# Optimization experiments

Measured on AMD Instinct MI355X. Metric: run time of the kernel, lower is better.

## Reference

```python
import jax, jax.numpy as jnp
import numpy as np

N = 100000
E = 1600000
H = 128       # hidden_channels
HEADS = 8
HD = H // HEADS  # head_dim = 16


def setup_inputs() -> dict:
    key = jax.random.key(0)
    ks = jax.random.split(key, 10)
    x = jax.random.normal(ks[0], (N, H), dtype=jnp.float32)
    gap_edge_index = jax.random.randint(ks[1], (2, E), 0, N, dtype=jnp.int64)
    s = 1.0 / np.sqrt(H)
    Wq = jax.random.normal(ks[2], (H, H), dtype=jnp.float32) * s
    bq = jnp.zeros((H,), dtype=jnp.float32)
    Wk = jax.random.normal(ks[3], (H, H), dtype=jnp.float32) * s
    bk = jnp.zeros((H,), dtype=jnp.float32)
    Wv = jax.random.normal(ks[4], (H, H), dtype=jnp.float32) * s
    bv = jnp.zeros((H,), dtype=jnp.float32)
    Wo = jax.random.normal(ks[5], (H, H), dtype=jnp.float32) * s
    bo = jnp.zeros((H,), dtype=jnp.float32)
    return {"x": x, "gap_edge_index": gap_edge_index,
            "Wq": Wq, "bq": bq, "Wk": Wk, "bk": bk,
            "Wv": Wv, "bv": bv, "Wo": Wo, "bo": bo}


def reference(x, gap_edge_index, Wq, bq, Wk, bk, Wv, bv, Wo, bo):
    n = x.shape[0]
    q = (x @ Wq + bq).reshape(n, HEADS, HD)
    k = (x @ Wk + bk).reshape(n, HEADS, HD)
    v = (x @ Wv + bv).reshape(n, HEADS, HD)
    src, dst = gap_edge_index[0], gap_edge_index[1]
    # per-edge, per-head scores: [E, heads]
    scores = jnp.einsum('ehd,ehd->eh', q[dst], k[src]) / jnp.sqrt(jnp.float32(HD))
    # NOTE: original softmaxes over ALL edges (dim=0), not per-dst segment
    w = jax.nn.softmax(scores, axis=0)
    # scatter-add weighted v[src] into dst: [N, heads, head_dim]
    attended = jax.ops.segment_sum(w[:, :, None] * v[src], dst, num_segments=n)
    attended = attended.reshape(n, HEADS * HD)
    return x + attended @ Wo + bo
```

## Files before the change

### kernel.cpp

```cpp
#include <hip/hip_runtime.h>
#include <cstdint>
#include <cstddef>

#define N_NODES 100000
#define E_EDGES 1600000
#define HCH 128
#define NHEADS 8
#define HDIM 16

typedef unsigned int uint;
typedef unsigned short ushort;
typedef __attribute__((ext_vector_type(8))) short short8;
typedef __attribute__((ext_vector_type(4))) float floatx4;
typedef __attribute__((ext_vector_type(2))) float floatx2;

typedef unsigned char uchar;

constexpr int GTILES = (N_NODES + 63) / 64;

__device__ __forceinline__ ushort f2bf(float f) {
    uint u = __float_as_uint(f);
    u = (u + 0x7fff + ((u >> 16) & 1)) >> 16;
    return (ushort)u;
}
__device__ __forceinline__ float bflo(uint p) { return __uint_as_float(p << 16); }
__device__ __forceinline__ float bfhi(uint p) { return __uint_as_float(p & 0xffff0000u); }

__global__ __launch_bounds__(256) void prep_w(
    const float* __restrict__ Wq, const float* __restrict__ Wk,
    const float* __restrict__ Wv, const float* __restrict__ Wo,
    ushort* __restrict__ wall)
{
    const int t = threadIdx.x;
    int r = blockIdx.x * 16 + (t >> 4);
    int k0 = (t & 15) * 8;
    const float* W;
    if (r < 128)      W = Wq;
    else if (r < 256) W = Wk;
    else if (r < 384) W = Wv;
    else              W = Wo;
    int n = r & 127;
    uint4 u;
    u.x = (uint)f2bf(W[(size_t)(k0 + 0) * HCH + n]) | ((uint)f2bf(W[(size_t)(k0 + 1) * HCH + n]) << 16);
    u.y = (uint)f2bf(W[(size_t)(k0 + 2) * HCH + n]) | ((uint)f2bf(W[(size_t)(k0 + 3) * HCH + n]) << 16);
    u.z = (uint)f2bf(W[(size_t)(k0 + 4) * HCH + n]) | ((uint)f2bf(W[(size_t)(k0 + 5) * HCH + n]) << 16);
    u.w = (uint)f2bf(W[(size_t)(k0 + 6) * HCH + n]) | ((uint)f2bf(W[(size_t)(k0 + 7) * HCH + n]) << 16);
    *(uint4*)(wall + (size_t)r * HCH + k0) = u;
}

__global__ __launch_bounds__(256) void gemm_qkv(
    const float* __restrict__ A, const ushort* __restrict__ wall,
    const float* __restrict__ bq, const float* __restrict__ bk, const float* __restrict__ bv,
    uchar* __restrict__ qe, uchar* __restrict__ kb, uchar* __restrict__ vb,
    int M)
{
    __shared__ __align__(16) ushort Wt[128][136];
    __shared__ __align__(16) char smem[64 * 136 * 2];
    ushort (*As)[136] = (ushort(*)[136])smem;
    ushort (*Cs)[136] = (ushort(*)[136])smem;

    const int t = threadIdx.x;
    const int mode = blockIdx.x % 3;
    const int tile0 = blockIdx.x / 3;
    const float* bias;
    uchar* outp;
    if (mode == 0)      { bias = bq; outp = qe; }
    else if (mode == 1) { bias = bk; outp = kb; }
    else                { bias = bv; outp = vb; }

#pragma unroll
    for (int i = 0; i < 8; i++) {
        int p = t + i * 256;
        int row = p >> 4, k0 = (p & 15) * 8;
        *(uint4*)(&Wt[row][k0]) =
            *(const uint4*)(wall + ((size_t)(mode * 128 + row)) * HCH + k0);
    }

    const int lane = t & 63;
    const int w = t >> 6;
    const int m_l = lane & 15;
    const int q_l = lane >> 4;

    for (int tile = tile0; tile < GTILES; tile += 256) {
        const int mb = tile * 64;
#pragma unroll
        for (int i = 0; i < 8; i++) {
            int p = t + i * 256;
            int row = p >> 5, c4 = p & 31;
            int g = mb + row;
            float4 a4 = make_float4(0.f, 0.f, 0.f, 0.f);
            if (g < M) a4 = *(const float4*)(A + (size_t)g * HCH + c4 * 4);
            uint lo = (uint)f2bf(a4.x) | ((uint)f2bf(a4.y) << 16);
            uint hi = (uint)f2bf(a4.z) | ((uint)f2bf(a4.w) << 16);
            *(uint2*)(&As[row][c4 * 4]) = make_uint2(lo, hi);
        }
        __syncthreads();

        floatx4 acc[8];
#pragma unroll
        for (int tl = 0; tl < 8; tl++) acc[tl] = (floatx4){0.f, 0.f, 0.f, 0.f};
#pragma unroll
        for (int ks = 0; ks < 4; ks++) {
            short8 af = *(const short8*)(&As[w * 16 + m_l][ks * 32 + q_l * 8]);
#pragma unroll
            for (int tl = 0; tl < 8; tl++) {
                short8 bf = *(const short8*)(&Wt[tl * 16 + m_l][ks * 32 + q_l * 8]);
                acc[tl] = __builtin_amdgcn_mfma_f32_16x16x32_bf16(af, bf, acc[tl], 0, 0, 0);
            }
        }
        __syncthreads();

#pragma unroll
        for (int tl = 0; tl < 8; tl++)
#pragma unroll
            for (int r = 0; r < 4; r++)
                Cs[w * 16 + q_l * 4 + r][tl * 16 + m_l] = f2bf(acc[tl][r]);
        __syncthreads();

#pragma unroll
        for (int i = 0; i < 4; i++) {
            int p = t + i * 256;
            int row = p >> 4, u = p & 15;
            int g = mb + row;
            if (g < M) {
                uint4 c = *(const uint4*)(&Cs[row][u * 8]);
                float4 b0 = *(const float4*)(bias + u * 8);
                float4 b1 = *(const float4*)(bias + u * 8 + 4);
                int r0 = __builtin_amdgcn_cvt_pk_fp8_f32(bflo(c.x) + b0.x, bfhi(c.x) + b0.y, 0, false);
                r0 = __builtin_amdgcn_cvt_pk_fp8_f32(bflo(c.y) + b0.z, bfhi(c.y) + b0.w, r0, true);
                int r1 = __builtin_amdgcn_cvt_pk_fp8_f32(bflo(c.z) + b1.x, bfhi(c.z) + b1.y, 0, false);
                r1 = __builtin_amdgcn_cvt_pk_fp8_f32(bflo(c.w) + b1.z, bfhi(c.w) + b1.w, r1, true);
                *(uint2*)(outp + (size_t)g * 128 + u * 8) = make_uint2((uint)r0, (uint)r1);
            }
        }
        __syncthreads();
    }
}

__global__ __launch_bounds__(256) void gemm_out(
    const ushort* __restrict__ A, const ushort* __restrict__ wall,
    const float* __restrict__ bias, const float* __restrict__ res,
    const float* __restrict__ head_invl,
    float* __restrict__ C, int M)
{
    __shared__ __align__(16) ushort Wt[128][136];
    __shared__ __align__(16) char smem[64 * 136 * 2];
    ushort (*As)[136] = (ushort(*)[136])smem;
    ushort (*Cs)[136] = (ushort(*)[136])smem;

    const int t = threadIdx.x;

    __shared__ float invl_s[8];
    if (t < 8) invl_s[t] = head_invl[t];

#pragma unroll
    for (int i = 0; i < 8; i++) {
        int p = t + i * 256;
        int row = p >> 4, k0 = (p & 15) * 8;
        *(uint4*)(&Wt[row][k0]) =
            *(const uint4*)(wall + ((size_t)(384 + row)) * HCH + k0);
    }

    const int lane = t & 63;
    const int w = t >> 6;
    const int m_l = lane & 15;
    const int q_l = lane >> 4;

    for (int tile = blockIdx.x; tile < GTILES; tile += 768) {
        const int mb = tile * 64;
#pragma unroll
        for (int i = 0; i < 8; i++) {
            int p = t + i * 256;
            int row = p >> 5, cu2 = p & 31;
            int g = mb + row;
            uint2 a = make_uint2(0, 0);
            if (g < M) a = *(const uint2*)(A + (size_t)g * HCH + cu2 * 4);
            float invl = invl_s[cu2 >> 2];
            float f0 = bflo(a.x) * invl, f1 = bfhi(a.x) * invl;
            float f2 = bflo(a.y) * invl, f3 = bfhi(a.y) * invl;
            uint lo = (uint)f2bf(f0) | ((uint)f2bf(f1) << 16);
            uint hi = (uint)f2bf(f2) | ((uint)f2bf(f3) << 16);
            *(uint2*)(&As[row][cu2 * 4]) = make_uint2(lo, hi);
        }
        __syncthreads();

        floatx4 acc[8];
#pragma unroll
        for (int tl = 0; tl < 8; tl++) acc[tl] = (floatx4){0.f, 0.f, 0.f, 0.f};
#pragma unroll
        for (int ks = 0; ks < 4; ks++) {
            short8 af = *(const short8*)(&As[w * 16 + m_l][ks * 32 + q_l * 8]);
#pragma unroll
            for (int tl = 0; tl < 8; tl++) {
                short8 bf = *(const short8*)(&Wt[tl * 16 + m_l][ks * 32 + q_l * 8]);
                acc[tl] = __builtin_amdgcn_mfma_f32_16x16x32_bf16(af, bf, acc[tl], 0, 0, 0);
            }
        }
        __syncthreads();

#pragma unroll
        for (int tl = 0; tl < 8; tl++)
#pragma unroll
            for (int r = 0; r < 4; r++)
                Cs[w * 16 + q_l * 4 + r][tl * 16 + m_l] = f2bf(acc[tl][r]);
        __syncthreads();

#pragma unroll
        for (int i = 0; i < 8; i++) {
            int p = t + i * 256;
            int row = p >> 5, u = p & 31;
            int g = mb + row;
            if (g < M) {
                uint2 c = *(const uint2*)(&Cs[row][u * 4]);
                float4 b4 = *(const float4*)(bias + u * 4);
                float4 r4 = *(const float4*)(res + (size_t)g * HCH + u * 4);
                float4 o;
                o.x = bflo(c.x) + b4.x + r4.x;
                o.y = bfhi(c.x) + b4.y + r4.y;
                o.z = bflo(c.y) + b4.z + r4.z;
                o.w = bfhi(c.y) + b4.w + r4.w;
                *(float4*)(C + (size_t)g * HCH + u * 4) = o;
            }
        }
        __syncthreads();
    }
}

constexpr int BSHIFT = 8;
constexpr int NBUCK  = ((N_NODES - 1) >> BSHIFT) + 1;
constexpr int S1_GRID = 256;
constexpr int S1_CH   = (E_EDGES + S1_GRID - 1) / S1_GRID;
constexpr int S2_CAP  = 6144;

__global__ __launch_bounds__(256) void bucket_hist(
    const int* __restrict__ dst, int* __restrict__ bucket_total)
{
    __shared__ int cnt[NBUCK];
    const int t = threadIdx.x;
    for (int b = t; b < NBUCK; b += 256) cnt[b] = 0;
    __syncthreads();
    const int e0 = blockIdx.x * S1_CH;
    const int n = min(S1_CH, E_EDGES - e0);
    for (int i = t; i < n; i += 256)
        atomicAdd(&cnt[dst[e0 + i] >> BSHIFT], 1);
    __syncthreads();
    for (int b = t; b < NBUCK; b += 256)
        if (cnt[b]) atomicAdd(&bucket_total[b], cnt[b]);
}

__global__ __launch_bounds__(512) void bucket_scan(
    const int* __restrict__ bucket_total, int* __restrict__ bucket_start,
    int* __restrict__ bucket_cursor, int* __restrict__ offsets)
{
    __shared__ int s[512];
    const int t = threadIdx.x;
    int v = (t < NBUCK) ? bucket_total[t] : 0;
    s[t] = v;
    __syncthreads();
    for (int off = 1; off < 512; off <<= 1) {
        int a = (t >= off) ? s[t - off] : 0;
        __syncthreads();
        s[t] += a;
        __syncthreads();
    }
    int excl = s[t] - v;
    if (t < NBUCK) { bucket_start[t] = excl; bucket_cursor[t] = excl; }
    if (t == 0) { bucket_start[NBUCK] = E_EDGES; offsets[N_NODES] = E_EDGES; }
}

__global__ __launch_bounds__(256) void sort_scatter1(
    const int* __restrict__ src, const int* __restrict__ dst,
    int* __restrict__ bucket_cursor, int2* __restrict__ tmp)
{
    __shared__ int ls[S1_CH];
    __shared__ int ld[S1_CH];
    __shared__ int cnt[NBUCK];
    const int t = threadIdx.x;
    for (int b = t; b < NBUCK; b += 256) cnt[b] = 0;
    __syncthreads();
    const int e0 = blockIdx.x * S1_CH;
    const int n = min(S1_CH, E_EDGES - e0);
    for (int i = t; i < n; i += 256) {
        int d = dst[e0 + i];
        ls[i] = src[e0 + i];
        ld[i] = d;
        atomicAdd(&cnt[d >> BSHIFT], 1);
    }
    __syncthreads();
    for (int b = t; b < NBUCK; b += 256) {
        int c = cnt[b];
        cnt[b] = c ? atomicAdd(&bucket_cursor[b], c) : 0;
    }
    __syncthreads();
    for (int i = t; i < n; i += 256) {
        int d = ld[i];
        int pos = atomicAdd(&cnt[d >> BSHIFT], 1);
        tmp[pos] = make_int2(ls[i], d);
    }
}

__global__ __launch_bounds__(256) void sort_scatter2(
    const int2* __restrict__ tmp, const int* __restrict__ bucket_start,
    int* __restrict__ psrc, int* __restrict__ offsets)
{
    __shared__ int2 le[S2_CAP];
    __shared__ int cnt[256];
    __shared__ int s[256];
    __shared__ int cur[256];
    const int t = threadIdx.x;
    const int b = blockIdx.x;
    const int bstart = bucket_start[b];
    const int n = bucket_start[b + 1] - bstart;
    cnt[t] = 0;
    __syncthreads();
    for (int i = t; i < n; i += 256) {
        int2 e = tmp[bstart + i];
        if (i < S2_CAP) le[i] = e;
        atomicAdd(&cnt[e.y & 255], 1);
    }
    __syncthreads();
    int v = cnt[t];
    s[t] = v;
    __syncthreads();
    for (int off = 1; off < 256; off <<= 1) {
        int a = (t >= off) ? s[t - off] : 0;
        __syncthreads();
        s[t] += a;
        __syncthreads();
    }
    int excl = s[t] - v;
    int node = (b << BSHIFT) + t;
    if (node < N_NODES) offsets[node] = bstart + excl;
    cur[t] = excl;
    __syncthreads();
    for (int i = t; i < n; i += 256) {
        int2 e = (i < S2_CAP) ? le[i] : tmp[bstart + i];
        int pos = bstart + atomicAdd(&cur[e.y & 255], 1);
        psrc[pos] = e.x;
    }
}

constexpr int FU_BLOCKS = 2048;
constexpr int FU_GROUPS = FU_BLOCKS * 16;

__device__ __forceinline__ float edge_w(
    uint2 e, floatx2 q0, floatx2 q1, floatx2 q2, floatx2 q3)
{
    floatx2 dp = q0 * __builtin_amdgcn_cvt_pk_f32_fp8((int)e.x, false);
    dp += q1 * __builtin_amdgcn_cvt_pk_f32_fp8((int)e.x, true);
    dp += q2 * __builtin_amdgcn_cvt_pk_f32_fp8((int)e.y, false);
    dp += q3 * __builtin_amdgcn_cvt_pk_f32_fp8((int)e.y, true);
    float p = dp.x + dp.y;
    p += __shfl_xor(p, 1);
    return __expf(p * 0.25f);
}
__device__ __forceinline__ void edge_acc(
    uint2 e, float wgt, floatx2& a01, floatx2& a23, floatx2& a45, floatx2& a67)
{
    floatx2 wv = {wgt, wgt};
    a01 += wv * __builtin_amdgcn_cvt_pk_f32_fp8((int)e.x, false);
    a23 += wv * __builtin_amdgcn_cvt_pk_f32_fp8((int)e.x, true);
    a45 += wv * __builtin_amdgcn_cvt_pk_f32_fp8((int)e.y, false);
    a67 += wv * __builtin_amdgcn_cvt_pk_f32_fp8((int)e.y, true);
}

__global__ __launch_bounds__(256) void edge_fused(
    const uchar* __restrict__ qe, const uchar* __restrict__ kb, const uchar* __restrict__ vb,
    const int* __restrict__ psrc, const int* __restrict__ offsets,
    ushort* __restrict__ attended, float* __restrict__ block_l)
{
    const int t = threadIdx.x;
    const int sub = t & 15;
    const int gg0 = blockIdx.x * 16 + (t >> 4);

    float lsum = 0.f;

    for (int d = gg0; d < N_NODES; d += FU_GROUPS) {
        const int start = offsets[d];
        const int end   = offsets[d + 1];

        uint2 qw = *(const uint2*)(qe + (size_t)d * 128 + sub * 8);
        floatx2 q0 = __builtin_amdgcn_cvt_pk_f32_fp8((int)qw.x, false);
        floatx2 q1 = __builtin_amdgcn_cvt_pk_f32_fp8((int)qw.x, true);
        floatx2 q2 = __builtin_amdgcn_cvt_pk_f32_fp8((int)qw.y, false);
        floatx2 q3 = __builtin_amdgcn_cvt_pk_f32_fp8((int)qw.y, true);

        floatx2 a01 = {0.f, 0.f}, a23 = {0.f, 0.f}, a45 = {0.f, 0.f}, a67 = {0.f, 0.f};

        for (int i = start; i < end; i += 4) {
            int i1 = min(i + 1, end - 1);
            int i2 = min(i + 2, end - 1);
            int i3 = min(i + 3, end - 1);
            int s0 = psrc[i];
            int s1 = psrc[i1];
            int s2 = psrc[i2];
            int s3 = psrc[i3];
            uint2 k0 = *(const uint2*)(kb + (size_t)s0 * 128 + sub * 8);
            uint2 k1 = *(const uint2*)(kb + (size_t)s1 * 128 + sub * 8);
            uint2 k2 = *(const uint2*)(kb + (size_t)s2 * 128 + sub * 8);
            uint2 k3 = *(const uint2*)(kb + (size_t)s3 * 128 + sub * 8);
            uint2 v0 = *(const uint2*)(vb + (size_t)s0 * 128 + sub * 8);
            uint2 v1 = *(const uint2*)(vb + (size_t)s1 * 128 + sub * 8);
            uint2 v2 = *(const uint2*)(vb + (size_t)s2 * 128 + sub * 8);
            uint2 v3 = *(const uint2*)(vb + (size_t)s3 * 128 + sub * 8);

            float w0 = edge_w(k0, q0, q1, q2, q3);
            float w1 = edge_w(k1, q0, q1, q2, q3);
            float w2 = edge_w(k2, q0, q1, q2, q3);
            float w3 = edge_w(k3, q0, q1, q2, q3);
            if (i + 1 >= end) w1 = 0.f;
            if (i + 2 >= end) w2 = 0.f;
            if (i + 3 >= end) w3 = 0.f;
            lsum += w0 + w1 + w2 + w3;

            edge_acc(v0, w0, a01, a23, a45, a67);
            edge_acc(v1, w1, a01, a23, a45, a67);
            edge_acc(v2, w2, a01, a23, a45, a67);
            edge_acc(v3, w3, a01, a23, a45, a67);
        }

        uint4 o;
        o.x = (uint)f2bf(a01.x) | ((uint)f2bf(a01.y) << 16);
        o.y = (uint)f2bf(a23.x) | ((uint)f2bf(a23.y) << 16);
        o.z = (uint)f2bf(a45.x) | ((uint)f2bf(a45.y) << 16);
        o.w = (uint)f2bf(a67.x) | ((uint)f2bf(a67.y) << 16);
        *(uint4*)(attended + (size_t)d * HCH + sub * 8) = o;
    }

    __shared__ float sl[256];
    sl[t] = lsum;
    __syncthreads();
    if (t < 8) {
        float L = 0.f;
        for (int base = 0; base < 256; base += 16)
            L += sl[base + 2 * t] + sl[base + 2 * t + 1];
        block_l[blockIdx.x * 8 + t] = 0.5f * L;
    }
}

__global__ __launch_bounds__(256) void reduce_l(
    const float* __restrict__ block_l, float* __restrict__ head_invl, int nblk)
{
    const int t = threadIdx.x;
    float l = 0.f;
    for (int i = t; i < nblk * 8; i += 256) l += block_l[i];
    __shared__ float sl[256];
    sl[t] = l;
    __syncthreads();
    if (t < 8) {
        float L = 0.f;
        for (int i = t; i < 256; i += 8) L += sl[i];
        head_invl[t] = 1.0f / L;
    }
}

extern "C" void kernel_launch(void* const* d_in, const int* in_sizes, int n_in,
                              void* d_out, int out_size, void* d_ws, size_t ws_size,
                              hipStream_t stream)
{
    const float* x  = (const float*)d_in[0];
    const int* eidx = (const int*)d_in[1];
    const float* Wq = (const float*)d_in[2];
    const float* bq = (const float*)d_in[3];
    const float* Wk = (const float*)d_in[4];
    const float* bk = (const float*)d_in[5];
    const float* Wv = (const float*)d_in[6];
    const float* bv = (const float*)d_in[7];
    const float* Wo = (const float*)d_in[8];
    const float* bo = (const float*)d_in[9];
    float* out = (float*)d_out;

    char* ws = (char*)d_ws;
    constexpr size_t SZ_F8  = (size_t)N_NODES * HCH;
    constexpr size_t SZ_ATT = (size_t)N_NODES * HCH * 2;
    constexpr size_t SZ_PS  = (size_t)E_EDGES * sizeof(int);
    constexpr size_t SZ_TMP = (size_t)E_EDGES * sizeof(int2);
    size_t off = 0;
    uchar* qe = (uchar*)(ws + off); off += SZ_F8;
    uchar* kb = (uchar*)(ws + off); off += SZ_F8;
    uchar* vb = (uchar*)(ws + off); off += SZ_F8;
    ushort* attended = (ushort*)(ws + off); off += SZ_ATT;
    int*    psrc     = (int*)(ws + off);    off += SZ_PS;
    int2*   tmp      = (int2*)(ws + off);   off += SZ_TMP;
    int*    offsets  = (int*)(ws + off);    off += ((size_t)N_NODES + 1) * 4 + 8;
    int*    bucket_total  = (int*)(ws + off); off += (NBUCK + 1) * 4;
    int*    bucket_start  = (int*)(ws + off); off += (NBUCK + 1) * 4;
    int*    bucket_cursor = (int*)(ws + off); off += (NBUCK + 1) * 4;
    float*  block_l   = (float*)(ws + off); off += (size_t)FU_BLOCKS * 8 * sizeof(float);
    float*  head_invl = (float*)(ws + off); off += 32;
    ushort* wall = (ushort*)(ws + off); off += (size_t)512 * HCH * 2;
    const int* src = eidx;
    const int* dst = eidx + E_EDGES;

    dim3 blk(256);

    prep_w<<<32, blk, 0, stream>>>(Wq, Wk, Wv, Wo, wall);

    gemm_qkv<<<768, blk, 0, stream>>>(x, wall, bq, bk, bv, qe, kb, vb, N_NODES);

    hipMemsetAsync(bucket_total, 0, (NBUCK + 1) * 4, stream);
    bucket_hist<<<S1_GRID, blk, 0, stream>>>(dst, bucket_total);
    bucket_scan<<<1, 512, 0, stream>>>(bucket_total, bucket_start, bucket_cursor, offsets);
    sort_scatter1<<<S1_GRID, blk, 0, stream>>>(src, dst, bucket_cursor, tmp);
    sort_scatter2<<<NBUCK, blk, 0, stream>>>(tmp, bucket_start, psrc, offsets);

    edge_fused<<<FU_BLOCKS, blk, 0, stream>>>(qe, kb, vb, psrc, offsets, attended, block_l);
    reduce_l<<<1, blk, 0, stream>>>(block_l, head_invl, FU_BLOCKS);

    gemm_out<<<768, blk, 0, stream>>>(attended, wall, bo, x, head_invl, out, N_NODES);
}
```

Measured before the change: 335.4 us.

## Fuse QKV GEMM with edge scatter, pack sort temp, prefetch tiles, drop launches

Merges the QKV projection GEMM and the first sort-scatter pass into one launch, with different block ranges doing different work so the two overlap. The sort temp is packed from int2 into a single uint holding the source id plus the low 8 bits of dst. Both GEMMs now register-prefetch the next A tile, and the edge loop double-buffers its K/V gathers. The memset and the reduce_l kernel are removed: bucket zeroing moves into prep_w and the softmax normaliser reduction moves into every gemm_out block. The trade-offs are redundant per-block reduction work and more register pressure. The packing also assumes source ids fit in 17 bits.

```diff
diff --git a/kernel.cpp b/kernel.cpp
--- a/kernel.cpp
+++ b/kernel.cpp
@@ -10,11 +10,10 @@
 
 typedef unsigned int uint;
 typedef unsigned short ushort;
+typedef unsigned char uchar;
 typedef __attribute__((ext_vector_type(8))) short short8;
 typedef __attribute__((ext_vector_type(4))) float floatx4;
 typedef __attribute__((ext_vector_type(2))) float floatx2;
-
-typedef unsigned char uchar;
 
 constexpr int GTILES = (N_NODES + 63) / 64;
 
@@ -26,12 +25,23 @@
 __device__ __forceinline__ float bflo(uint p) { return __uint_as_float(p << 16); }
 __device__ __forceinline__ float bfhi(uint p) { return __uint_as_float(p & 0xffff0000u); }
 
+constexpr int BSHIFT = 8;
+constexpr int NBUCK  = ((N_NODES - 1) >> BSHIFT) + 1;
+constexpr int S1_GRID = 256;
+constexpr int S1_CH   = (E_EDGES + S1_GRID - 1) / S1_GRID;
+constexpr int S2_CAP  = 6144;
+constexpr int FU_BLOCKS = 2048;
+constexpr int FU_GROUPS = FU_BLOCKS * 16;
+
 __global__ __launch_bounds__(256) void prep_w(
     const float* __restrict__ Wq, const float* __restrict__ Wk,
     const float* __restrict__ Wv, const float* __restrict__ Wo,
-    ushort* __restrict__ wall)
-{
-    const int t = threadIdx.x;
+    ushort* __restrict__ wall, int* __restrict__ bucket_total)
+{
+    const int t = threadIdx.x;
+    if (blockIdx.x == 0) {
+        for (int b = t; b < NBUCK + 1; b += 256) bucket_total[b] = 0;
+    }
     int r = blockIdx.x * 16 + (t >> 4);
     int k0 = (t & 15) * 8;
     const float* W;
@@ -48,20 +58,84 @@
     *(uint4*)(wall + (size_t)r * HCH + k0) = u;
 }
 
-__global__ __launch_bounds__(256) void gemm_qkv(
+__global__ __launch_bounds__(256) void bucket_hist(
+    const int* __restrict__ dst, int* __restrict__ bucket_total)
+{
+    __shared__ int cnt[NBUCK];
+    const int t = threadIdx.x;
+    for (int b = t; b < NBUCK; b += 256) cnt[b] = 0;
+    __syncthreads();
+    const int e0 = blockIdx.x * S1_CH;
+    const int n = min(S1_CH, E_EDGES - e0);
+    for (int i = t; i < n; i += 256)
+        atomicAdd(&cnt[dst[e0 + i] >> BSHIFT], 1);
+    __syncthreads();
+    for (int b = t; b < NBUCK; b += 256)
+        if (cnt[b]) atomicAdd(&bucket_total[b], cnt[b]);
+}
+
+__global__ __launch_bounds__(512) void bucket_scan(
+    const int* __restrict__ bucket_total, int* __restrict__ bucket_start,
+    int* __restrict__ bucket_cursor, int* __restrict__ offsets)
+{
+    __shared__ int s[512];
+    const int t = threadIdx.x;
+    int v = (t < NBUCK) ? bucket_total[t] : 0;
+    s[t] = v;
+    __syncthreads();
+    for (int off = 1; off < 512; off <<= 1) {
+        int a = (t >= off) ? s[t - off] : 0;
+        __syncthreads();
+        s[t] += a;
+        __syncthreads();
+    }
+    int excl = s[t] - v;
+    if (t < NBUCK) { bucket_start[t] = excl; bucket_cursor[t] = excl; }
+    if (t == 0) { bucket_start[NBUCK] = E_EDGES; offsets[N_NODES] = E_EDGES; }
+}
+
+__global__ __launch_bounds__(256) void mega_qkv_scatter(
     const float* __restrict__ A, const ushort* __restrict__ wall,
     const float* __restrict__ bq, const float* __restrict__ bk, const float* __restrict__ bv,
     uchar* __restrict__ qe, uchar* __restrict__ kb, uchar* __restrict__ vb,
+    const int* __restrict__ src, const int* __restrict__ dst,
+    int* __restrict__ bucket_cursor, uint* __restrict__ tmp,
     int M)
 {
-    __shared__ __align__(16) ushort Wt[128][136];
-    __shared__ __align__(16) char smem[64 * 136 * 2];
-    ushort (*As)[136] = (ushort(*)[136])smem;
-    ushort (*Cs)[136] = (ushort(*)[136])smem;
-
-    const int t = threadIdx.x;
-    const int mode = blockIdx.x % 3;
-    const int tile0 = blockIdx.x / 3;
+    __shared__ __align__(16) char sm[34816 + 17408];
+    const int t = threadIdx.x;
+    const int bid = blockIdx.x;
+
+    if (bid < S1_GRID) {
+        int* cnt = (int*)sm;
+        for (int b = t; b < NBUCK; b += 256) cnt[b] = 0;
+        __syncthreads();
+        const int e0 = bid * S1_CH;
+        const int n = min(S1_CH, E_EDGES - e0);
+        for (int i = t; i < n; i += 256)
+            atomicAdd(&cnt[dst[e0 + i] >> BSHIFT], 1);
+        __syncthreads();
+        for (int b = t; b < NBUCK; b += 256) {
+            int c = cnt[b];
+            cnt[b] = c ? atomicAdd(&bucket_cursor[b], c) : 0;
+        }
+        __syncthreads();
+        for (int i = t; i < n; i += 256) {
+            int d = dst[e0 + i];
+            int s = src[e0 + i];
+            int pos = atomicAdd(&cnt[d >> BSHIFT], 1);
+            tmp[pos] = (uint)s | ((uint)(d & 255) << 24);
+        }
+        return;
+    }
+
+    ushort (*Wt)[136] = (ushort(*)[136])sm;
+    ushort (*As)[136] = (ushort(*)[136])(sm + 34816);
+    ushort (*Cs)[136] = (ushort(*)[136])(sm + 34816);
+
+    const int b = bid - S1_GRID;
+    const int mode = b % 3;
+    const int tile0 = b / 3;
     const float* bias;
     uchar* outp;
     if (mode == 0)      { bias = bq; outp = qe; }
@@ -81,18 +155,41 @@
     const int m_l = lane & 15;
     const int q_l = lane >> 4;
 
+    const int eu = t & 15;
+    const float4 eb0 = *(const float4*)(bias + eu * 8);
+    const float4 eb1 = *(const float4*)(bias + eu * 8 + 4);
+    const int arow = t >> 5, ac4 = t & 31;
+
+    float4 a4[8];
+    {
+        const int mb = tile0 * 64;
+#pragma unroll
+        for (int i = 0; i < 8; i++) {
+            int row = arow + i * 8;
+            int g = mb + row;
+            a4[i] = make_float4(0.f, 0.f, 0.f, 0.f);
+            if (g < M) a4[i] = *(const float4*)(A + (size_t)g * HCH + ac4 * 4);
+        }
+    }
+
     for (int tile = tile0; tile < GTILES; tile += 256) {
         const int mb = tile * 64;
 #pragma unroll
         for (int i = 0; i < 8; i++) {
-            int p = t + i * 256;
-            int row = p >> 5, c4 = p & 31;
-            int g = mb + row;
-            float4 a4 = make_float4(0.f, 0.f, 0.f, 0.f);
-            if (g < M) a4 = *(const float4*)(A + (size_t)g * HCH + c4 * 4);
-            uint lo = (uint)f2bf(a4.x) | ((uint)f2bf(a4.y) << 16);
-            uint hi = (uint)f2bf(a4.z) | ((uint)f2bf(a4.w) << 16);
-            *(uint2*)(&As[row][c4 * 4]) = make_uint2(lo, hi);
+            uint lo = (uint)f2bf(a4[i].x) | ((uint)f2bf(a4[i].y) << 16);
+            uint hi = (uint)f2bf(a4[i].z) | ((uint)f2bf(a4[i].w) << 16);
+            *(uint2*)(&As[arow + i * 8][ac4 * 4]) = make_uint2(lo, hi);
+        }
+        const int ntile = tile + 256;
+        if (ntile < GTILES) {
+            const int nmb = ntile * 64;
+#pragma unroll
+            for (int i = 0; i < 8; i++) {
+                int g = nmb + arow + i * 8;
+                float4 v = make_float4(0.f, 0.f, 0.f, 0.f);
+                if (g < M) v = *(const float4*)(A + (size_t)g * HCH + ac4 * 4);
+                a4[i] = v;
+            }
         }
         __syncthreads();
 
@@ -119,191 +216,26 @@
 
 #pragma unroll
         for (int i = 0; i < 4; i++) {
-            int p = t + i * 256;
-            int row = p >> 4, u = p & 15;
+            int row = (t >> 4) + i * 16;
             int g = mb + row;
             if (g < M) {
-                uint4 c = *(const uint4*)(&Cs[row][u * 8]);
-                float4 b0 = *(const float4*)(bias + u * 8);
-                float4 b1 = *(const float4*)(bias + u * 8 + 4);
-                int r0 = __builtin_amdgcn_cvt_pk_fp8_f32(bflo(c.x) + b0.x, bfhi(c.x) + b0.y, 0, false);
-                r0 = __builtin_amdgcn_cvt_pk_fp8_f32(bflo(c.y) + b0.z, bfhi(c.y) + b0.w, r0, true);
-                int r1 = __builtin_amdgcn_cvt_pk_fp8_f32(bflo(c.z) + b1.x, bfhi(c.z) + b1.y, 0, false);
-                r1 = __builtin_amdgcn_cvt_pk_fp8_f32(bflo(c.w) + b1.z, bfhi(c.w) + b1.w, r1, true);
-                *(uint2*)(outp + (size_t)g * 128 + u * 8) = make_uint2((uint)r0, (uint)r1);
-            }
-        }
-        __syncthreads();
-    }
-}
-
-__global__ __launch_bounds__(256) void gemm_out(
-    const ushort* __restrict__ A, const ushort* __restrict__ wall,
-    const float* __restrict__ bias, const float* __restrict__ res,
-    const float* __restrict__ head_invl,
-    float* __restrict__ C, int M)
-{
-    __shared__ __align__(16) ushort Wt[128][136];
-    __shared__ __align__(16) char smem[64 * 136 * 2];
-    ushort (*As)[136] = (ushort(*)[136])smem;
-    ushort (*Cs)[136] = (ushort(*)[136])smem;
-
-    const int t = threadIdx.x;
-
-    __shared__ float invl_s[8];
-    if (t < 8) invl_s[t] = head_invl[t];
-
-#pragma unroll
-    for (int i = 0; i < 8; i++) {
-        int p = t + i * 256;
-        int row = p >> 4, k0 = (p & 15) * 8;
-        *(uint4*)(&Wt[row][k0]) =
-            *(const uint4*)(wall + ((size_t)(384 + row)) * HCH + k0);
-    }
-
-    const int lane = t & 63;
-    const int w = t >> 6;
-    const int m_l = lane & 15;
-    const int q_l = lane >> 4;
-
-    for (int tile = blockIdx.x; tile < GTILES; tile += 768) {
-        const int mb = tile * 64;
-#pragma unroll
-        for (int i = 0; i < 8; i++) {
-            int p = t + i * 256;
-            int row = p >> 5, cu2 = p & 31;
-            int g = mb + row;
-            uint2 a = make_uint2(0, 0);
-            if (g < M) a = *(const uint2*)(A + (size_t)g * HCH + cu2 * 4);
-            float invl = invl_s[cu2 >> 2];
-            float f0 = bflo(a.x) * invl, f1 = bfhi(a.x) * invl;
-            float f2 = bflo(a.y) * invl, f3 = bfhi(a.y) * invl;
-            uint lo = (uint)f2bf(f0) | ((uint)f2bf(f1) << 16);
-            uint hi = (uint)f2bf(f2) | ((uint)f2bf(f3) << 16);
-            *(uint2*)(&As[row][cu2 * 4]) = make_uint2(lo, hi);
-        }
-        __syncthreads();
-
-        floatx4 acc[8];
-#pragma unroll
-        for (int tl = 0; tl < 8; tl++) acc[tl] = (floatx4){0.f, 0.f, 0.f, 0.f};
-#pragma unroll
-        for (int ks = 0; ks < 4; ks++) {
-            short8 af = *(const short8*)(&As[w * 16 + m_l][ks * 32 + q_l * 8]);
-#pragma unroll
-            for (int tl = 0; tl < 8; tl++) {
-                short8 bf = *(const short8*)(&Wt[tl * 16 + m_l][ks * 32 + q_l * 8]);
-                acc[tl] = __builtin_amdgcn_mfma_f32_16x16x32_bf16(af, bf, acc[tl], 0, 0, 0);
-            }
-        }
-        __syncthreads();
-
-#pragma unroll
-        for (int tl = 0; tl < 8; tl++)
-#pragma unroll
-            for (int r = 0; r < 4; r++)
-                Cs[w * 16 + q_l * 4 + r][tl * 16 + m_l] = f2bf(acc[tl][r]);
-        __syncthreads();
-
-#pragma unroll
-        for (int i = 0; i < 8; i++) {
-            int p = t + i * 256;
-            int row = p >> 5, u = p & 31;
-            int g = mb + row;
-            if (g < M) {
-                uint2 c = *(const uint2*)(&Cs[row][u * 4]);
-                float4 b4 = *(const float4*)(bias + u * 4);
-                float4 r4 = *(const float4*)(res + (size_t)g * HCH + u * 4);
-                float4 o;
-                o.x = bflo(c.x) + b4.x + r4.x;
-                o.y = bfhi(c.x) + b4.y + r4.y;
-                o.z = bflo(c.y) + b4.z + r4.z;
-                o.w = bfhi(c.y) + b4.w + r4.w;
-                *(float4*)(C + (size_t)g * HCH + u * 4) = o;
-            }
-        }
-        __syncthreads();
-    }
-}
-
-constexpr int BSHIFT = 8;
-constexpr int NBUCK  = ((N_NODES - 1) >> BSHIFT) + 1;
-constexpr int S1_GRID = 256;
-constexpr int S1_CH   = (E_EDGES + S1_GRID - 1) / S1_GRID;
-constexpr int S2_CAP  = 6144;
-
-__global__ __launch_bounds__(256) void bucket_hist(
-    const int* __restrict__ dst, int* __restrict__ bucket_total)
-{
-    __shared__ int cnt[NBUCK];
-    const int t = threadIdx.x;
-    for (int b = t; b < NBUCK; b += 256) cnt[b] = 0;
-    __syncthreads();
-    const int e0 = blockIdx.x * S1_CH;
-    const int n = min(S1_CH, E_EDGES - e0);
-    for (int i = t; i < n; i += 256)
-        atomicAdd(&cnt[dst[e0 + i] >> BSHIFT], 1);
-    __syncthreads();
-    for (int b = t; b < NBUCK; b += 256)
-        if (cnt[b]) atomicAdd(&bucket_total[b], cnt[b]);
-}
-
-__global__ __launch_bounds__(512) void bucket_scan(
-    const int* __restrict__ bucket_total, int* __restrict__ bucket_start,
-    int* __restrict__ bucket_cursor, int* __restrict__ offsets)
-{
-    __shared__ int s[512];
-    const int t = threadIdx.x;
-    int v = (t < NBUCK) ? bucket_total[t] : 0;
-    s[t] = v;
-    __syncthreads();
-    for (int off = 1; off < 512; off <<= 1) {
-        int a = (t >= off) ? s[t - off] : 0;
-        __syncthreads();
-        s[t] += a;
-        __syncthreads();
-    }
-    int excl = s[t] - v;
-    if (t < NBUCK) { bucket_start[t] = excl; bucket_cursor[t] = excl; }
-    if (t == 0) { bucket_start[NBUCK] = E_EDGES; offsets[N_NODES] = E_EDGES; }
-}
-
-__global__ __launch_bounds__(256) void sort_scatter1(
-    const int* __restrict__ src, const int* __restrict__ dst,
-    int* __restrict__ bucket_cursor, int2* __restrict__ tmp)
-{
-    __shared__ int ls[S1_CH];
-    __shared__ int ld[S1_CH];
-    __shared__ int cnt[NBUCK];
-    const int t = threadIdx.x;
-    for (int b = t; b < NBUCK; b += 256) cnt[b] = 0;
-    __syncthreads();
-    const int e0 = blockIdx.x * S1_CH;
-    const int n = min(S1_CH, E_EDGES - e0);
-    for (int i = t; i < n; i += 256) {
-        int d = dst[e0 + i];
-        ls[i] = src[e0 + i];
-        ld[i] = d;
-        atomicAdd(&cnt[d >> BSHIFT], 1);
-    }
-    __syncthreads();
-    for (int b = t; b < NBUCK; b += 256) {
-        int c = cnt[b];
-        cnt[b] = c ? atomicAdd(&bucket_cursor[b], c) : 0;
-    }
-    __syncthreads();
-    for (int i = t; i < n; i += 256) {
-        int d = ld[i];
-        int pos = atomicAdd(&cnt[d >> BSHIFT], 1);
-        tmp[pos] = make_int2(ls[i], d);
+                uint4 c = *(const uint4*)(&Cs[row][eu * 8]);
+                int r0 = __builtin_amdgcn_cvt_pk_fp8_f32(bflo(c.x) + eb0.x, bfhi(c.x) + eb0.y, 0, false);
+                r0 = __builtin_amdgcn_cvt_pk_fp8_f32(bflo(c.y) + eb0.z, bfhi(c.y) + eb0.w, r0, true);
+                int r1 = __builtin_amdgcn_cvt_pk_fp8_f32(bflo(c.z) + eb1.x, bfhi(c.z) + eb1.y, 0, false);
+                r1 = __builtin_amdgcn_cvt_pk_fp8_f32(bflo(c.w) + eb1.z, bfhi(c.w) + eb1.w, r1, true);
+                *(uint2*)(outp + (size_t)g * 128 + eu * 8) = make_uint2((uint)r0, (uint)r1);
+            }
+        }
+        __syncthreads();
     }
 }
 
 __global__ __launch_bounds__(256) void sort_scatter2(
-    const int2* __restrict__ tmp, const int* __restrict__ bucket_start,
+    const uint* __restrict__ tmp, const int* __restrict__ bucket_start,
     int* __restrict__ psrc, int* __restrict__ offsets)
 {
-    __shared__ int2 le[S2_CAP];
+    __shared__ uint le[S2_CAP];
     __shared__ int cnt[256];
     __shared__ int s[256];
     __shared__ int cur[256];
@@ -314,9 +246,9 @@
     cnt[t] = 0;
     __syncthreads();
     for (int i = t; i < n; i += 256) {
-        int2 e = tmp[bstart + i];
+        uint e = tmp[bstart + i];
         if (i < S2_CAP) le[i] = e;
-        atomicAdd(&cnt[e.y & 255], 1);
+        atomicAdd(&cnt[e >> 24], 1);
     }
     __syncthreads();
     int v = cnt[t];
@@ -334,14 +266,11 @@
     cur[t] = excl;
     __syncthreads();
     for (int i = t; i < n; i += 256) {
-        int2 e = (i < S2_CAP) ? le[i] : tmp[bstart + i];
-        int pos = bstart + atomicAdd(&cur[e.y & 255], 1);
-        psrc[pos] = e.x;
-    }
-}
-
-constexpr int FU_BLOCKS = 2048;
-constexpr int FU_GROUPS = FU_BLOCKS * 16;
+        uint e = (i < S2_CAP) ? le[i] : tmp[bstart + i];
+        int pos = bstart + atomicAdd(&cur[e >> 24], 1);
+        psrc[pos] = (int)(e & 0x1FFFFu);
+    }
+}
 
 __device__ __forceinline__ float edge_w(
     uint2 e, floatx2 q0, floatx2 q1, floatx2 q2, floatx2 q3)
@@ -364,6 +293,36 @@
     a67 += wv * __builtin_amdgcn_cvt_pk_f32_fp8((int)e.y, true);
 }
 
+#define LOADQ(S, base) do { \
+    int jj1 = min((base) + 1, end - 1); \
+    int jj2 = min((base) + 2, end - 1); \
+    int jj3 = min((base) + 3, end - 1); \
+    int u0 = psrc[(base)], u1 = psrc[jj1], u2 = psrc[jj2], u3 = psrc[jj3]; \
+    k##S##0 = *(const uint2*)(kb + (size_t)u0 * 128 + sub * 8); \
+    k##S##1 = *(const uint2*)(kb + (size_t)u1 * 128 + sub * 8); \
+    k##S##2 = *(const uint2*)(kb + (size_t)u2 * 128 + sub * 8); \
+    k##S##3 = *(const uint2*)(kb + (size_t)u3 * 128 + sub * 8); \
+    v##S##0 = *(const uint2*)(vb + (size_t)u0 * 128 + sub * 8); \
+    v##S##1 = *(const uint2*)(vb + (size_t)u1 * 128 + sub * 8); \
+    v##S##2 = *(const uint2*)(vb + (size_t)u2 * 128 + sub * 8); \
+    v##S##3 = *(const uint2*)(vb + (size_t)u3 * 128 + sub * 8); \
+} while (0)
+
+#define COMPQ(S, base) do { \
+    float w0 = edge_w(k##S##0, q0, q1, q2, q3); \
+    float w1 = edge_w(k##S##1, q0, q1, q2, q3); \
+    float w2 = edge_w(k##S##2, q0, q1, q2, q3); \
+    float w3 = edge_w(k##S##3, q0, q1, q2, q3); \
+    if ((base) + 1 >= end) w1 = 0.f; \
+    if ((base) + 2 >= end) w2 = 0.f; \
+    if ((base) + 3 >= end) w3 = 0.f; \
+    lsum += w0 + w1 + w2 + w3; \
+    edge_acc(v##S##0, w0, a01, a23, a45, a67); \
+    edge_acc(v##S##1, w1, a01, a23, a45, a67); \
+    edge_acc(v##S##2, w2, a01, a23, a45, a67); \
+    edge_acc(v##S##3, w3, a01, a23, a45, a67); \
+} while (0)
+
 __global__ __launch_bounds__(256) void edge_fused(
     const uchar* __restrict__ qe, const uchar* __restrict__ kb, const uchar* __restrict__ vb,
     const int* __restrict__ psrc, const int* __restrict__ offsets,
@@ -387,36 +346,22 @@
 
         floatx2 a01 = {0.f, 0.f}, a23 = {0.f, 0.f}, a45 = {0.f, 0.f}, a67 = {0.f, 0.f};
 
-        for (int i = start; i < end; i += 4) {
-            int i1 = min(i + 1, end - 1);
-            int i2 = min(i + 2, end - 1);
-            int i3 = min(i + 3, end - 1);
-            int s0 = psrc[i];
-            int s1 = psrc[i1];
-            int s2 = psrc[i2];
-            int s3 = psrc[i3];
-            uint2 k0 = *(const uint2*)(kb + (size_t)s0 * 128 + sub * 8);
-            uint2 k1 = *(const uint2*)(kb + (size_t)s1 * 128 + sub * 8);
-            uint2 k2 = *(const uint2*)(kb + (size_t)s2 * 128 + sub * 8);
-            uint2 k3 = *(const uint2*)(kb + (size_t)s3 * 128 + sub * 8);
-            uint2 v0 = *(const uint2*)(vb + (size_t)s0 * 128 + sub * 8);
-            uint2 v1 = *(const uint2*)(vb + (size_t)s1 * 128 + sub * 8);
-            uint2 v2 = *(const uint2*)(vb + (size_t)s2 * 128 + sub * 8);
-            uint2 v3 = *(const uint2*)(vb + (size_t)s3 * 128 + sub * 8);
-
-            float w0 = edge_w(k0, q0, q1, q2, q3);
-            float w1 = edge_w(k1, q0, q1, q2, q3);
-            float w2 = edge_w(k2, q0, q1, q2, q3);
-            float w3 = edge_w(k3, q0, q1, q2, q3);
-            if (i + 1 >= end) w1 = 0.f;
-            if (i + 2 >= end) w2 = 0.f;
-            if (i + 3 >= end) w3 = 0.f;
-            lsum += w0 + w1 + w2 + w3;
-
-            edge_acc(v0, w0, a01, a23, a45, a67);
-            edge_acc(v1, w1, a01, a23, a45, a67);
-            edge_acc(v2, w2, a01, a23, a45, a67);
-            edge_acc(v3, w3, a01, a23, a45, a67);
+        uint2 kA0, kA1, kA2, kA3, vA0, vA1, vA2, vA3;
+        uint2 kB0, kB1, kB2, kB3, vB0, vB1, vB2, vB3;
+
+        int i = start;
+        if (i < end) {
+            LOADQ(A, i);
+            while (true) {
+                if (i + 4 < end) LOADQ(B, i + 4);
+                COMPQ(A, i);
+                i += 4;
+                if (i >= end) break;
+                if (i + 4 < end) LOADQ(A, i + 4);
+                COMPQ(B, i);
+                i += 4;
+                if (i >= end) break;
+            }
         }
 
         uint4 o;
@@ -438,19 +383,123 @@
     }
 }
 
-__global__ __launch_bounds__(256) void reduce_l(
-    const float* __restrict__ block_l, float* __restrict__ head_invl, int nblk)
-{
-    const int t = threadIdx.x;
-    float l = 0.f;
-    for (int i = t; i < nblk * 8; i += 256) l += block_l[i];
+__global__ __launch_bounds__(256) void gemm_out(
+    const ushort* __restrict__ A, const ushort* __restrict__ wall,
+    const float* __restrict__ bias, const float* __restrict__ res,
+    const float* __restrict__ block_l,
+    float* __restrict__ C, int M)
+{
+    __shared__ __align__(16) char sm[34816 + 17408];
+    ushort (*Wt)[136] = (ushort(*)[136])sm;
+    ushort (*As)[136] = (ushort(*)[136])(sm + 34816);
+    ushort (*Cs)[136] = (ushort(*)[136])(sm + 34816);
+    __shared__ float invl_s[8];
     __shared__ float sl[256];
-    sl[t] = l;
-    __syncthreads();
-    if (t < 8) {
-        float L = 0.f;
-        for (int i = t; i < 256; i += 8) L += sl[i];
-        head_invl[t] = 1.0f / L;
+
+    const int t = threadIdx.x;
+
+    {
+        float l = 0.f;
+        for (int i = t; i < FU_BLOCKS * 8; i += 256) l += block_l[i];
+        sl[t] = l;
+        __syncthreads();
+        if (t < 8) {
+            float L = 0.f;
+            for (int j = t; j < 256; j += 8) L += sl[j];
+            invl_s[t] = 1.0f / L;
+        }
+    }
+
+#pragma unroll
+    for (int i = 0; i < 8; i++) {
+        int p = t + i * 256;
+        int row = p >> 4, k0 = (p & 15) * 8;
+        *(uint4*)(&Wt[row][k0]) =
+            *(const uint4*)(wall + ((size_t)(384 + row)) * HCH + k0);
+    }
+    __syncthreads();
+
+    const int lane = t & 63;
+    const int w = t >> 6;
+    const int m_l = lane & 15;
+    const int q_l = lane >> 4;
+
+    const int arow = t >> 5, acu2 = t & 31;
+    const float invl_a = invl_s[acu2 >> 2];
+    const int eu = t & 31;
+    const float4 eb = *(const float4*)(bias + eu * 4);
+
+    uint2 a2[8];
+    {
+        const int mb = blockIdx.x * 64;
+#pragma unroll
+        for (int i = 0; i < 8; i++) {
+            int g = mb + arow + i * 8;
+            a2[i] = make_uint2(0, 0);
+            if (g < M) a2[i] = *(const uint2*)(A + (size_t)g * HCH + acu2 * 4);
+        }
+    }
+
+    for (int tile = blockIdx.x; tile < GTILES; tile += 768) {
+        const int mb = tile * 64;
+#pragma unroll
+        for (int i = 0; i < 8; i++) {
+            float f0 = bflo(a2[i].x) * invl_a, f1 = bfhi(a2[i].x) * invl_a;
+            float f2 = bflo(a2[i].y) * invl_a, f3 = bfhi(a2[i].y) * invl_a;
+            uint lo = (uint)f2bf(f0) | ((uint)f2bf(f1) << 16);
+            uint hi = (uint)f2bf(f2) | ((uint)f2bf(f3) << 16);
+            *(uint2*)(&As[arow + i * 8][acu2 * 4]) = make_uint2(lo, hi);
+        }
+        const int ntile = tile + 768;
+        if (ntile < GTILES) {
+            const int nmb = ntile * 64;
+#pragma unroll
+            for (int i = 0; i < 8; i++) {
+                int g = nmb + arow + i * 8;
+                uint2 v = make_uint2(0, 0);
+                if (g < M) v = *(const uint2*)(A + (size_t)g * HCH + acu2 * 4);
+                a2[i] = v;
+            }
+        }
+        __syncthreads();
+
+        floatx4 acc[8];
+#pragma unroll
+        for (int tl = 0; tl < 8; tl++) acc[tl] = (floatx4){0.f, 0.f, 0.f, 0.f};
+#pragma unroll
+        for (int ks = 0; ks < 4; ks++) {
+            short8 af = *(const short8*)(&As[w * 16 + m_l][ks * 32 + q_l * 8]);
+#pragma unroll
+            for (int tl = 0; tl < 8; tl++) {
+                short8 bf = *(const short8*)(&Wt[tl * 16 + m_l][ks * 32 + q_l * 8]);
+                acc[tl] = __builtin_amdgcn_mfma_f32_16x16x32_bf16(af, bf, acc[tl], 0, 0, 0);
+            }
+        }
+        __syncthreads();
+
+#pragma unroll
+        for (int tl = 0; tl < 8; tl++)
+#pragma unroll
+            for (int r = 0; r < 4; r++)
+                Cs[w * 16 + q_l * 4 + r][tl * 16 + m_l] = f2bf(acc[tl][r]);
+        __syncthreads();
+
+#pragma unroll
+        for (int i = 0; i < 8; i++) {
+            int row = (t >> 5) + i * 8;
+            int g = mb + row;
+            if (g < M) {
+                uint2 c = *(const uint2*)(&Cs[row][eu * 4]);
+                float4 r4 = *(const float4*)(res + (size_t)g * HCH + eu * 4);
+                float4 o;
+                o.x = bflo(c.x) + eb.x + r4.x;
+                o.y = bfhi(c.x) + eb.y + r4.y;
+                o.z = bflo(c.y) + eb.z + r4.z;
+                o.w = bfhi(c.y) + eb.w + r4.w;
+                *(float4*)(C + (size_t)g * HCH + eu * 4) = o;
+            }
+        }
+        __syncthreads();
     }
 }
 
@@ -474,38 +523,35 @@
     constexpr size_t SZ_F8  = (size_t)N_NODES * HCH;
     constexpr size_t SZ_ATT = (size_t)N_NODES * HCH * 2;
     constexpr size_t SZ_PS  = (size_t)E_EDGES * sizeof(int);
-    constexpr size_t SZ_TMP = (size_t)E_EDGES * sizeof(int2);
+    constexpr size_t SZ_TMP = (size_t)E_EDGES * sizeof(uint);
     size_t off = 0;
     uchar* qe = (uchar*)(ws + off); off += SZ_F8;
     uchar* kb = (uchar*)(ws + off); off += SZ_F8;
     uchar* vb = (uchar*)(ws + off); off += SZ_F8;
     ushort* attended = (ushort*)(ws + off); off += SZ_ATT;
     int*    psrc     = (int*)(ws + off);    off += SZ_PS;
-    int2*   tmp      = (int2*)(ws + off);   off += SZ_TMP;
+    uint*   tmp      = (uint*)(ws + off);   off += SZ_TMP;
     int*    offsets  = (int*)(ws + off);    off += ((size_t)N_NODES + 1) * 4 + 8;
     int*    bucket_total  = (int*)(ws + off); off += (NBUCK + 1) * 4;
     int*    bucket_start  = (int*)(ws + off); off += (NBUCK + 1) * 4;
     int*    bucket_cursor = (int*)(ws + off); off += (NBUCK + 1) * 4;
     float*  block_l   = (float*)(ws + off); off += (size_t)FU_BLOCKS * 8 * sizeof(float);
-    float*  head_invl = (float*)(ws + off); off += 32;
     ushort* wall = (ushort*)(ws + off); off += (size_t)512 * HCH * 2;
     const int* src = eidx;
     const int* dst = eidx + E_EDGES;
 
     dim3 blk(256);
 
-    prep_w<<<32, blk, 0, stream>>>(Wq, Wk, Wv, Wo, wall);
-
-    gemm_qkv<<<768, blk, 0, stream>>>(x, wall, bq, bk, bv, qe, kb, vb, N_NODES);
-
-    hipMemsetAsync(bucket_total, 0, (NBUCK + 1) * 4, stream);
+    prep_w<<<32, blk, 0, stream>>>(Wq, Wk, Wv, Wo, wall, bucket_total);
     bucket_hist<<<S1_GRID, blk, 0, stream>>>(dst, bucket_total);
     bucket_scan<<<1, 512, 0, stream>>>(bucket_total, bucket_start, bucket_cursor, offsets);
-    sort_scatter1<<<S1_GRID, blk, 0, stream>>>(src, dst, bucket_cursor, tmp);
+
+    mega_qkv_scatter<<<S1_GRID + 768, blk, 0, stream>>>(
+        x, wall, bq, bk, bv, qe, kb, vb, src, dst, bucket_cursor, tmp, N_NODES);
+
     sort_scatter2<<<NBUCK, blk, 0, stream>>>(tmp, bucket_start, psrc, offsets);
 
     edge_fused<<<FU_BLOCKS, blk, 0, stream>>>(qe, kb, vb, psrc, offsets, attended, block_l);
-    reduce_l<<<1, blk, 0, stream>>>(block_l, head_invl, FU_BLOCKS);
-
-    gemm_out<<<768, blk, 0, stream>>>(attended, wall, bo, x, head_invl, out, N_NODES);
-}
+
+    gemm_out<<<768, blk, 0, stream>>>(attended, wall, bo, x, block_l, out, N_NODES);
+}
```

Result: faster. 295.9 us (-11.8%).
